# Kernel tuning notes

Hardware: AMD Instinct MI355X
Metric: run time of the kernel (lower is better)

The kernel has to match this reference:

```python
import jax, jax.numpy as jnp
import numpy as np

B, S, E, D, OUT = 128, 128, 256, 256, 64


def setup_inputs() -> dict:
    key = jax.random.key(0)
    ks = jax.random.split(key, 10)
    w = lambda k, shp, s=0.05: (jax.random.normal(k, shp, dtype=jnp.float32) * s)
    return {
        "input_encoded": jax.random.normal(ks[0], (B, S, E), dtype=jnp.float32),
        "y_history": jax.random.normal(ks[1], (B, S, OUT), dtype=jnp.float32),
        "h0": jax.random.normal(ks[2], (B, D), dtype=jnp.float32) * 0.1,
        "c0": jax.random.normal(ks[3], (B, D), dtype=jnp.float32) * 0.1,
        "attn_W1": w(ks[4], (2 * D + E, E)),
        "attn_b1": jnp.zeros((E,), jnp.float32),
        "attn_w2": w(ks[5], (E,)),
        "attn_b2": jnp.zeros((1,), jnp.float32),
        "lstm_Wih": w(ks[6], (OUT, 4 * D)),
        "lstm_Whh": w(ks[7], (D, 4 * D)),
        "lstm_bih": jnp.zeros((4 * D,), jnp.float32),
        "lstm_bhh": jnp.zeros((4 * D,), jnp.float32),
        "fc_W": w(ks[8], (E + OUT, OUT)),
        "fc_b": jnp.zeros((OUT,), jnp.float32),
        "fc_out_W": w(ks[9], (D + E, OUT * S)),
        "fc_out_b": jnp.zeros((OUT * S,), jnp.float32),
    }


def reference(input_encoded, y_history, h0, c0, attn_W1, attn_b1, attn_w2, attn_b2,
              lstm_Wih, lstm_Whh, lstm_bih, lstm_bhh, fc_W, fc_b, fc_out_W, fc_out_b):
    # Split the attn first-layer weight according to the concat order (h, c, enc).
    Wh, Wc, We = attn_W1[:D], attn_W1[D:2 * D], attn_W1[2 * D:]
    # Encoder projection is time-invariant across decoder steps; hoist it.
    enc_proj = jnp.einsum('bse,ef->bsf', input_encoded, We)  # [B,S,E]

    def step(carry, y_t):
        h, c, _ = carry
        hc = h @ Wh + c @ Wc + attn_b1                       # [B,E]
        pre = jnp.tanh(enc_proj + hc[:, None, :])            # [B,S,E]
        scores = pre @ attn_w2 + attn_b2[0]                  # [B,S]
        alpha = jax.nn.softmax(scores, axis=1)
        context = jnp.einsum('bs,bse->be', alpha, input_encoded)  # [B,E]
        y_tilde = jnp.concatenate([context, y_t], axis=1) @ fc_W + fc_b  # [B,OUT]
        gates = y_tilde @ lstm_Wih + lstm_bih + h @ lstm_Whh + lstm_bhh  # [B,4D]
        i, f, g, o = jnp.split(gates, 4, axis=1)  # pytorch gate order i,f,g,o
        c_new = jax.nn.sigmoid(f) * c + jax.nn.sigmoid(i) * jnp.tanh(g)
        h_new = jax.nn.sigmoid(o) * jnp.tanh(c_new)
        return (h_new, c_new, context), None

    y_seq = jnp.transpose(y_history, (1, 0, 2))  # [S,B,OUT]
    (h_T, c_T, context_T), _ = jax.lax.scan(step, (h0, c0, jnp.zeros((B, E), h0.dtype)), y_seq)
    out = jnp.concatenate([h_T, context_T], axis=1) @ fc_out_W + fc_out_b  # [B,OUT*S]
    return out.reshape(-1, S, OUT)
```

## Files before the change

kernel.cpp:

```cpp
#include <hip/hip_runtime.h>

#define BB 128
#define SS 128
#define EE 256
#define DD 256
#define OO 64

#define W1_OFF   0
#define WHH_OFF  196608
#define WIH_OFF  458752
#define FCW_OFF  524288
#define WTOTAL   544768

__device__ __forceinline__ float fsig(float x) { return 1.0f / (1.0f + __expf(-x)); }
__device__ __forceinline__ float ftanh(float x) {
    float t = __expf(-2.0f * fabsf(x));
    float r = (1.0f - t) / (1.0f + t);
    return copysignf(r, x);
}
__device__ __forceinline__ int SWZ(int e) { return (e & ~31) | ((e + 4 * (e >> 5)) & 31); }
__device__ __forceinline__ float bflo(unsigned int u) { return __uint_as_float(u << 16); }
__device__ __forceinline__ float bfhi(unsigned int u) { return __uint_as_float(u & 0xffff0000u); }

__device__ __forceinline__ void fma8(const uint4 w, const float xv, float* acc) {
    acc[0] += xv * bflo(w.x); acc[1] += xv * bfhi(w.x);
    acc[2] += xv * bflo(w.y); acc[3] += xv * bfhi(w.y);
    acc[4] += xv * bflo(w.z); acc[5] += xv * bfhi(w.z);
    acc[6] += xv * bflo(w.w); acc[7] += xv * bfhi(w.w);
}

__global__ __launch_bounds__(256) void conv_kernel(
    const float* __restrict__ W1, const float* __restrict__ Whh,
    const float* __restrict__ Wih, const float* __restrict__ fcW,
    unsigned short* __restrict__ out)
{
    const int idx = blockIdx.x * 256 + threadIdx.x;
    float f;
    if      (idx < WHH_OFF)  f = W1[idx];
    else if (idx < WIH_OFF)  f = Whh[idx - WHH_OFF];
    else if (idx < FCW_OFF)  f = Wih[idx - WIH_OFF];
    else if (idx < WTOTAL)   f = fcW[idx - FCW_OFF];
    else return;
    unsigned int u = __float_as_uint(f);
    u = (u + 0x7fffu + ((u >> 16) & 1u)) >> 16;
    out[idx] = (unsigned short)u;
}

__global__ __launch_bounds__(1024, 4) void scan_kernel(
    const float* __restrict__ inp,
    const float* __restrict__ yhist,
    const float* __restrict__ h0, const float* __restrict__ c0,
    const float* __restrict__ W1f,
    const float* __restrict__ b1, const float* __restrict__ w2, const float* __restrict__ b2,
    const float* __restrict__ bih, const float* __restrict__ bhh,
    const float* __restrict__ fcb,
    const unsigned short* __restrict__ wbf,
    float* __restrict__ hctxT)
{
    __shared__ float sh_inp[SS * 260];
    __shared__ float red1[16 * 256];
    __shared__ float sh_bs[1024];
    __shared__ float sh_h[DD], sh_c[DD];
    __shared__ float sh_hc[EE];
    __shared__ float sh_w2[EE];
    __shared__ float sh_raw[SS];
    __shared__ float sh_ctx[EE];
    __shared__ float sh_y[OO], sh_yt[OO];
    __shared__ float sh_misc[1];

    const int b = blockIdx.x, t = threadIdx.x;
    const float* inp_b = inp + (size_t)b * SS * EE;
    const unsigned short* W1bf  = wbf + W1_OFF;
    const unsigned short* Whhbf = wbf + WHH_OFF;
    const unsigned short* Wihbf = wbf + WIH_OFF;
    const unsigned short* fcWbf = wbf + FCW_OFF;
    const float b2v = b2[0];
    const int lane = t & 63;

    const int e8 = (t & 31) * 8, kc1 = t >> 5;
    const int cg2 = t >> 3, kg2 = t & 7;
    const int s_own = t >> 3, a2 = t & 7, e0 = a2 * 32;
    const int e4 = (t & 63) * 4, sg3 = t >> 6;
    const int kf = (t & 63) * 5, cf = (t >> 6) * 4;

    #pragma unroll
    for (int i = 0; i < 8; ++i) {
        const int idx = i * 1024 + t;
        const int s = idx >> 6, c4 = (idx & 63) * 4;
        *(float4*)&sh_inp[s * 260 + c4] = *(const float4*)(inp_b + (size_t)idx * 4);
    }
    if (t < 256) {
        sh_h[t] = h0[b * 256 + t]; sh_c[t] = c0[b * 256 + t];
        sh_w2[SWZ(t)] = w2[t];
    }
    sh_bs[t] = bih[t] + bhh[t];

    uint4 wih_r[8];
    #pragma unroll
    for (int i = 0; i < 8; ++i)
        wih_r[i] = *(const uint4*)(Wihbf + (size_t)(kg2 * 8 + i) * 1024 + cg2 * 8);
    uint2 fcw_r[5];
    #pragma unroll
    for (int i = 0; i < 5; ++i)
        fcw_r[i] = *(const uint2*)(fcWbf + (kf + i) * 64 + cf);
    __syncthreads();

    float er[32];
    #pragma unroll
    for (int j = 0; j < 32; ++j) er[j] = 0.f;
    {
        const float* We = W1f + 512 * 256;
        for (int kc = 0; kc < 16; ++kc) {
            {
                const int row = t >> 6, c4 = (t & 63) * 4;
                *(float4*)&red1[row * 256 + c4] =
                    *(const float4*)(We + (size_t)(kc * 16 + row) * 256 + c4);
            }
            __syncthreads();
            for (int k = 0; k < 16; ++k) {
                const float xv = sh_inp[s_own * 260 + kc * 16 + k];
                #pragma unroll
                for (int j4 = 0; j4 < 8; ++j4) {
                    float4 w = *(const float4*)&red1[k * 256 + e0 + j4 * 4];
                    er[j4*4+0] += xv * w.x; er[j4*4+1] += xv * w.y;
                    er[j4*4+2] += xv * w.z; er[j4*4+3] += xv * w.w;
                }
            }
            __syncthreads();
        }
        if (t < 256) red1[t] = b1[t];
        __syncthreads();
        #pragma unroll
        for (int j4 = 0; j4 < 8; ++j4) {
            float4 v = *(const float4*)&red1[e0 + j4 * 4];
            er[j4*4+0] += v.x; er[j4*4+1] += v.y; er[j4*4+2] += v.z; er[j4*4+3] += v.w;
        }
        __syncthreads();
    }

    for (int ts = 0; ts < SS; ++ts) {
        if (t < 64) sh_y[t] = yhist[(size_t)b * SS * OO + ts * OO + t];

        {
            float acc[8];
            #pragma unroll
            for (int r = 0; r < 8; ++r) acc[r] = 0.f;
            #pragma unroll 4
            for (int k = kc1 * 16; k < kc1 * 16 + 16; ++k) {
                const float xv = (k < 256) ? sh_h[k] : sh_c[k - 256];
                uint4 w = *(const uint4*)(W1bf + (size_t)k * 256 + e8);
                fma8(w, xv, acc);
            }
            #pragma unroll
            for (int r = 0; r < 8; ++r) acc[r] += __shfl_xor(acc[r], 32);
            if ((t & 32) == 0) {
                *(float4*)&red1[(kc1 >> 1) * 256 + e8]     = make_float4(acc[0], acc[1], acc[2], acc[3]);
                *(float4*)&red1[(kc1 >> 1) * 256 + e8 + 4] = make_float4(acc[4], acc[5], acc[6], acc[7]);
            }
        }
        __syncthreads();
        if (t < 256) {
            float v = 0.f;
            #pragma unroll
            for (int r = 0; r < 16; ++r) v += red1[r * 256 + t];
            sh_hc[SWZ(t)] = v;
        }
        __syncthreads();

        float g[8];
        #pragma unroll
        for (int r = 0; r < 8; ++r) g[r] = 0.f;
        #pragma unroll 8
        for (int i = 0; i < 32; ++i) {
            const int k = kg2 * 32 + ((i + 4 * kg2) & 31);
            const float hv = sh_h[k];
            uint4 w = *(const uint4*)(Whhbf + (size_t)k * 1024 + cg2 * 8);
            fma8(w, hv, g);
        }
        {
            float sacc = 0.f;
            #pragma unroll
            for (int j4 = 0; j4 < 8; ++j4) {
                const int phys = e0 + ((j4 * 4 + 4 * a2) & 31);
                float4 hc4 = *(const float4*)&sh_hc[phys];
                float4 w24 = *(const float4*)&sh_w2[phys];
                sacc += ftanh(er[j4*4+0] + hc4.x) * w24.x;
                sacc += ftanh(er[j4*4+1] + hc4.y) * w24.y;
                sacc += ftanh(er[j4*4+2] + hc4.z) * w24.z;
                sacc += ftanh(er[j4*4+3] + hc4.w) * w24.w;
            }
            sacc += __shfl_xor(sacc, 1);
            sacc += __shfl_xor(sacc, 2);
            sacc += __shfl_xor(sacc, 4);
            if (a2 == 0) sh_raw[s_own] = __expf(sacc + b2v);
        }
        __syncthreads();

        {
            float ax = 0.f, ay = 0.f, az = 0.f, aw = 0.f;
            #pragma unroll
            for (int i = 0; i < 8; ++i) {
                const int s = sg3 * 8 + i;
                const float al = sh_raw[s];
                float4 iv = *(const float4*)&sh_inp[s * 260 + e4];
                ax += al * iv.x; ay += al * iv.y; az += al * iv.z; aw += al * iv.w;
            }
            *(float4*)&red1[sg3 * 256 + e4] = make_float4(ax, ay, az, aw);
        }
        if (t < 64) {
            float v = sh_raw[t] + sh_raw[t + 64];
            #pragma unroll
            for (int m = 32; m > 0; m >>= 1) v += __shfl_xor(v, m);
            if (t == 0) sh_misc[0] = 1.0f / v;
        }
        __syncthreads();
        if (t < 256) {
            float v = 0.f;
            #pragma unroll
            for (int r = 0; r < 16; ++r) v += red1[r * 256 + t];
            v *= sh_misc[0];
            sh_ctx[t] = v;
            if (ts == SS - 1) hctxT[(size_t)(256 + t) * 128 + b] = v;
        }
        __syncthreads();

        {
            float a0 = 0.f, a1 = 0.f, a2v = 0.f, a3 = 0.f;
            #pragma unroll
            for (int i = 0; i < 5; ++i) {
                const int k = kf + i;
                const float val = (k < 256) ? sh_ctx[k] : sh_y[k - 256];
                const uint2 w = fcw_r[i];
                a0  += val * bflo(w.x); a1 += val * bfhi(w.x);
                a2v += val * bflo(w.y); a3 += val * bfhi(w.y);
            }
            #pragma unroll
            for (int m = 1; m < 64; m <<= 1) {
                a0  += __shfl_xor(a0, m);  a1 += __shfl_xor(a1, m);
                a2v += __shfl_xor(a2v, m); a3 += __shfl_xor(a3, m);
            }
            if (lane == 0) {
                float4 r; r.x = a0 + fcb[cf]; r.y = a1 + fcb[cf + 1];
                r.z = a2v + fcb[cf + 2]; r.w = a3 + fcb[cf + 3];
                *(float4*)&sh_yt[cf] = r;
            }
        }
        __syncthreads();

        #pragma unroll
        for (int i = 0; i < 8; ++i) {
            const float yv = sh_yt[kg2 * 8 + i];
            fma8(wih_r[i], yv, g);
        }
        #pragma unroll
        for (int r = 0; r < 8; ++r) {
            g[r] += __shfl_xor(g[r], 1);
            g[r] += __shfl_xor(g[r], 2);
            g[r] += __shfl_xor(g[r], 4);
        }
        if (kg2 == 0) {
            *(float4*)&red1[cg2 * 8]     = make_float4(g[0], g[1], g[2], g[3]);
            *(float4*)&red1[cg2 * 8 + 4] = make_float4(g[4], g[5], g[6], g[7]);
        }
        __syncthreads();
        if (t < 256) {
            const float gi = red1[t]       + sh_bs[t];
            const float gf = red1[256 + t] + sh_bs[256 + t];
            const float gg = red1[512 + t] + sh_bs[512 + t];
            const float go = red1[768 + t] + sh_bs[768 + t];
            const float cn = fsig(gf) * sh_c[t] + fsig(gi) * ftanh(gg);
            sh_c[t] = cn;
            const float hn = fsig(go) * ftanh(cn);
            sh_h[t] = hn;
            if (ts == SS - 1) hctxT[(size_t)t * 128 + b] = hn;
        }
        __syncthreads();
    }
}

__global__ __launch_bounds__(256) void out_gemm(
    const float* __restrict__ AT, const float* __restrict__ W,
    const float* __restrict__ bias, float* __restrict__ out)
{
    __shared__ float Ab[64 * 132];
    __shared__ float Bb[64 * 32];
    const int t = threadIdx.x;
    const int nt = blockIdx.x * 32;
    const int n4 = (t & 7) * 4;
    const int m4 = (t >> 3) * 4;
    float acc[4][4];
    #pragma unroll
    for (int i = 0; i < 4; ++i)
        #pragma unroll
        for (int jj = 0; jj < 4; ++jj) acc[i][jj] = 0.f;

    for (int kc = 0; kc < 8; ++kc) {
        #pragma unroll
        for (int i = 0; i < 8; ++i) {
            const int flat4 = i * 256 + t;
            const int row = flat4 >> 5, mm4 = (flat4 & 31) * 4;
            float4 v = *(const float4*)(AT + (size_t)(kc * 64 + row) * 128 + mm4);
            *(float4*)&Ab[row * 132 + mm4] = v;
        }
        #pragma unroll
        for (int i = 0; i < 2; ++i) {
            const int fl = t + i * 256;
            const int k = fl >> 3, nn4 = (fl & 7) * 4;
            *(float4*)&Bb[k * 32 + nn4] =
                *(const float4*)(W + (size_t)(kc * 64 + k) * 8192 + nt + nn4);
        }
        __syncthreads();
        for (int k = 0; k < 64; ++k) {
            const float4 bv = *(const float4*)&Bb[k * 32 + n4];
            const float4 av = *(const float4*)&Ab[k * 132 + m4];
            acc[0][0] += av.x * bv.x; acc[0][1] += av.x * bv.y; acc[0][2] += av.x * bv.z; acc[0][3] += av.x * bv.w;
            acc[1][0] += av.y * bv.x; acc[1][1] += av.y * bv.y; acc[1][2] += av.y * bv.z; acc[1][3] += av.y * bv.w;
            acc[2][0] += av.z * bv.x; acc[2][1] += av.z * bv.y; acc[2][2] += av.z * bv.z; acc[2][3] += av.z * bv.w;
            acc[3][0] += av.w * bv.x; acc[3][1] += av.w * bv.y; acc[3][2] += av.w * bv.z; acc[3][3] += av.w * bv.w;
        }
        __syncthreads();
    }
    const float4 bb = *(const float4*)(bias + nt + n4);
    #pragma unroll
    for (int i = 0; i < 4; ++i) {
        float4 r;
        r.x = acc[i][0] + bb.x; r.y = acc[i][1] + bb.y;
        r.z = acc[i][2] + bb.z; r.w = acc[i][3] + bb.w;
        *(float4*)(out + (size_t)(m4 + i) * 8192 + nt + n4) = r;
    }
}

extern "C" void kernel_launch(void* const* d_in, const int* in_sizes, int n_in,
                              void* d_out, int out_size, void* d_ws, size_t ws_size,
                              hipStream_t stream) {
    const float* inp = (const float*)d_in[0];
    const float* yh  = (const float*)d_in[1];
    const float* h0  = (const float*)d_in[2];
    const float* c0  = (const float*)d_in[3];
    const float* W1  = (const float*)d_in[4];
    const float* b1  = (const float*)d_in[5];
    const float* w2  = (const float*)d_in[6];
    const float* b2  = (const float*)d_in[7];
    const float* Wih = (const float*)d_in[8];
    const float* Whh = (const float*)d_in[9];
    const float* bih = (const float*)d_in[10];
    const float* bhh = (const float*)d_in[11];
    const float* fcW = (const float*)d_in[12];
    const float* fcb = (const float*)d_in[13];
    const float* foW = (const float*)d_in[14];
    const float* fob = (const float*)d_in[15];

    float* hctxT = (float*)d_ws;
    unsigned short* wbf = (unsigned short*)d_out;

    conv_kernel<<<dim3((WTOTAL + 255) / 256), dim3(256), 0, stream>>>(W1, Whh, Wih, fcW, wbf);
    scan_kernel<<<dim3(BB), dim3(1024), 0, stream>>>(
        inp, yh, h0, c0, W1, b1, w2, b2, bih, bhh, fcb, wbf, hctxT);
    out_gemm<<<dim3(8192 / 32), dim3(256), 0, stream>>>(hctxT, foW, fob, (float*)d_out);
}
```

Measured before the change: 5.483 ms.

## Halve scan block to 512 threads and keep encoder projection in LDS

The recurrent scan kernel now runs with 512 threads per batch row instead of 1024. The precomputed encoder projection plus bias is stored in shared memory rather than held in registers, while the raw input for the context sum is read from global/L2. All four partitions of the matmuls are reworked: deeper per-thread K loops, Wih and fcW weights streamed each step instead of kept in registers, and gate bias folded into the initial accumulators. The aim is fewer threads and shuffles per barrier in this latency-bound serial loop. The cost is more sequential work per thread, an extra barrier in the fc stage, and the context sum now reading inputs from global memory on every step.

```diff
diff --git a/kernel.cpp b/kernel.cpp
--- a/kernel.cpp
+++ b/kernel.cpp
@@ -18,7 +18,6 @@
     float r = (1.0f - t) / (1.0f + t);
     return copysignf(r, x);
 }
-__device__ __forceinline__ int SWZ(int e) { return (e & ~31) | ((e + 4 * (e >> 5)) & 31); }
 __device__ __forceinline__ float bflo(unsigned int u) { return __uint_as_float(u << 16); }
 __device__ __forceinline__ float bfhi(unsigned int u) { return __uint_as_float(u & 0xffff0000u); }
 
@@ -46,7 +45,7 @@
     out[idx] = (unsigned short)u;
 }
 
-__global__ __launch_bounds__(1024, 4) void scan_kernel(
+__global__ __launch_bounds__(512, 2) void scan_kernel(
     const float* __restrict__ inp,
     const float* __restrict__ yhist,
     const float* __restrict__ h0, const float* __restrict__ c0,
@@ -57,16 +56,14 @@
     const unsigned short* __restrict__ wbf,
     float* __restrict__ hctxT)
 {
-    __shared__ float sh_inp[SS * 260];
-    __shared__ float red1[16 * 256];
-    __shared__ float sh_bs[1024];
+    __shared__ float sh_enc[SS * 260];
+    __shared__ float red1a[4096];
+    __shared__ float red1b[1024];
     __shared__ float sh_h[DD], sh_c[DD];
-    __shared__ float sh_hc[EE];
-    __shared__ float sh_w2[EE];
-    __shared__ float sh_raw[SS];
+    __shared__ float sh_hc[EE], sh_w2[EE];
+    __shared__ float sh_raw[132];
     __shared__ float sh_ctx[EE];
     __shared__ float sh_y[OO], sh_yt[OO];
-    __shared__ float sh_misc[1];
 
     const int b = blockIdx.x, t = threadIdx.x;
     const float* inp_b = inp + (size_t)b * SS * EE;
@@ -75,202 +72,195 @@
     const unsigned short* Wihbf = wbf + WIH_OFF;
     const unsigned short* fcWbf = wbf + FCW_OFF;
     const float b2v = b2[0];
-    const int lane = t & 63;
-
-    const int e8 = (t & 31) * 8, kc1 = t >> 5;
-    const int cg2 = t >> 3, kg2 = t & 7;
-    const int s_own = t >> 3, a2 = t & 7, e0 = a2 * 32;
-    const int e4 = (t & 63) * 4, sg3 = t >> 6;
-    const int kf = (t & 63) * 5, cf = (t >> 6) * 4;
-
-    #pragma unroll
-    for (int i = 0; i < 8; ++i) {
-        const int idx = i * 1024 + t;
-        const int s = idx >> 6, c4 = (idx & 63) * 4;
-        *(float4*)&sh_inp[s * 260 + c4] = *(const float4*)(inp_b + (size_t)idx * 4);
-    }
+
+    const int kc1 = t >> 5, e8 = (t & 31) * 8;
+    const int kc2 = t >> 7, j8 = (t & 127) * 8;
+    const int s_own = t >> 2, a2 = t & 3;
+    const int sg3 = t >> 7, c2 = (t & 127) * 2;
+    const int kg = t >> 5, c2b = (t & 31) * 2;
+
     if (t < 256) {
         sh_h[t] = h0[b * 256 + t]; sh_c[t] = c0[b * 256 + t];
-        sh_w2[SWZ(t)] = w2[t];
-    }
-    sh_bs[t] = bih[t] + bhh[t];
-
-    uint4 wih_r[8];
+        sh_w2[t] = w2[t];
+        sh_hc[t] = b1[t];
+    }
+    float bs_r[8];
     #pragma unroll
-    for (int i = 0; i < 8; ++i)
-        wih_r[i] = *(const uint4*)(Wihbf + (size_t)(kg2 * 8 + i) * 1024 + cg2 * 8);
-    uint2 fcw_r[5];
-    #pragma unroll
-    for (int i = 0; i < 5; ++i)
-        fcw_r[i] = *(const uint2*)(fcWbf + (kf + i) * 64 + cf);
+    for (int r = 0; r < 8; ++r) bs_r[r] = 0.f;
+    if (t < 128) {
+        #pragma unroll
+        for (int r = 0; r < 8; ++r) bs_r[r] = bih[t * 8 + r] + bhh[t * 8 + r];
+    }
+    const float fcb_reg = (t < 64) ? fcb[t] : 0.f;
     __syncthreads();
 
-    float er[32];
-    #pragma unroll
-    for (int j = 0; j < 32; ++j) er[j] = 0.f;
     {
+        float4 ec[16];
+        #pragma unroll
+        for (int d = 0; d < 16; ++d) ec[d] = make_float4(0.f, 0.f, 0.f, 0.f);
         const float* We = W1f + 512 * 256;
         for (int kc = 0; kc < 16; ++kc) {
             {
-                const int row = t >> 6, c4 = (t & 63) * 4;
-                *(float4*)&red1[row * 256 + c4] =
-                    *(const float4*)(We + (size_t)(kc * 16 + row) * 256 + c4);
-            }
+                const int row = t >> 5, c8 = (t & 31) * 8;
+                *(float4*)&red1a[row * 256 + c8] =
+                    *(const float4*)(We + (size_t)(kc * 16 + row) * 256 + c8);
+                *(float4*)&red1a[row * 256 + c8 + 4] =
+                    *(const float4*)(We + (size_t)(kc * 16 + row) * 256 + c8 + 4);
+            }
+            float4 xq = *(const float4*)(inp_b + (size_t)s_own * 256 + kc * 16 + a2 * 4);
             __syncthreads();
-            for (int k = 0; k < 16; ++k) {
-                const float xv = sh_inp[s_own * 260 + kc * 16 + k];
+            #pragma unroll
+            for (int q = 0; q < 4; ++q) {
+                const int src = (t & 60) | q;
+                float4 xs;
+                xs.x = __shfl(xq.x, src, 64); xs.y = __shfl(xq.y, src, 64);
+                xs.z = __shfl(xq.z, src, 64); xs.w = __shfl(xq.w, src, 64);
+                const float xv[4] = {xs.x, xs.y, xs.z, xs.w};
                 #pragma unroll
-                for (int j4 = 0; j4 < 8; ++j4) {
-                    float4 w = *(const float4*)&red1[k * 256 + e0 + j4 * 4];
-                    er[j4*4+0] += xv * w.x; er[j4*4+1] += xv * w.y;
-                    er[j4*4+2] += xv * w.z; er[j4*4+3] += xv * w.w;
+                for (int j = 0; j < 4; ++j) {
+                    const int krow = q * 4 + j;
+                    #pragma unroll
+                    for (int d = 0; d < 16; ++d) {
+                        float4 w = *(const float4*)&red1a[krow * 256 + a2 * 64 + d * 4];
+                        ec[d].x += xv[j] * w.x; ec[d].y += xv[j] * w.y;
+                        ec[d].z += xv[j] * w.z; ec[d].w += xv[j] * w.w;
+                    }
                 }
             }
             __syncthreads();
         }
-        if (t < 256) red1[t] = b1[t];
-        __syncthreads();
-        #pragma unroll
-        for (int j4 = 0; j4 < 8; ++j4) {
-            float4 v = *(const float4*)&red1[e0 + j4 * 4];
-            er[j4*4+0] += v.x; er[j4*4+1] += v.y; er[j4*4+2] += v.z; er[j4*4+3] += v.w;
+        #pragma unroll
+        for (int d = 0; d < 16; ++d) {
+            float4 bv = *(const float4*)&sh_hc[a2 * 64 + d * 4];
+            float4 v;
+            v.x = ec[d].x + bv.x; v.y = ec[d].y + bv.y;
+            v.z = ec[d].z + bv.z; v.w = ec[d].w + bv.w;
+            *(float4*)&sh_enc[s_own * 260 + a2 * 64 + d * 4] = v;
         }
         __syncthreads();
     }
 
     for (int ts = 0; ts < SS; ++ts) {
-        if (t < 64) sh_y[t] = yhist[(size_t)b * SS * OO + ts * OO + t];
-
         {
             float acc[8];
             #pragma unroll
             for (int r = 0; r < 8; ++r) acc[r] = 0.f;
-            #pragma unroll 4
-            for (int k = kc1 * 16; k < kc1 * 16 + 16; ++k) {
+            #pragma unroll 8
+            for (int k = kc1 * 32; k < kc1 * 32 + 32; ++k) {
                 const float xv = (k < 256) ? sh_h[k] : sh_c[k - 256];
                 uint4 w = *(const uint4*)(W1bf + (size_t)k * 256 + e8);
                 fma8(w, xv, acc);
             }
-            #pragma unroll
-            for (int r = 0; r < 8; ++r) acc[r] += __shfl_xor(acc[r], 32);
-            if ((t & 32) == 0) {
-                *(float4*)&red1[(kc1 >> 1) * 256 + e8]     = make_float4(acc[0], acc[1], acc[2], acc[3]);
-                *(float4*)&red1[(kc1 >> 1) * 256 + e8 + 4] = make_float4(acc[4], acc[5], acc[6], acc[7]);
-            }
-        }
+            *(float4*)&red1a[kc1 * 256 + e8]     = make_float4(acc[0], acc[1], acc[2], acc[3]);
+            *(float4*)&red1a[kc1 * 256 + e8 + 4] = make_float4(acc[4], acc[5], acc[6], acc[7]);
+        }
+        if (t >= 448) sh_y[t - 448] = yhist[(size_t)b * SS * OO + ts * OO + (t - 448)];
         __syncthreads();
         if (t < 256) {
             float v = 0.f;
             #pragma unroll
-            for (int r = 0; r < 16; ++r) v += red1[r * 256 + t];
-            sh_hc[SWZ(t)] = v;
+            for (int r = 0; r < 16; ++r) v += red1a[r * 256 + t];
+            sh_hc[t] = v;
         }
         __syncthreads();
 
         float g[8];
         #pragma unroll
-        for (int r = 0; r < 8; ++r) g[r] = 0.f;
+        for (int r = 0; r < 8; ++r) g[r] = bs_r[r];
         #pragma unroll 8
-        for (int i = 0; i < 32; ++i) {
-            const int k = kg2 * 32 + ((i + 4 * kg2) & 31);
+        for (int k = kc2 * 64; k < kc2 * 64 + 64; ++k) {
             const float hv = sh_h[k];
-            uint4 w = *(const uint4*)(Whhbf + (size_t)k * 1024 + cg2 * 8);
+            uint4 w = *(const uint4*)(Whhbf + (size_t)k * 1024 + j8);
             fma8(w, hv, g);
         }
         {
             float sacc = 0.f;
             #pragma unroll
-            for (int j4 = 0; j4 < 8; ++j4) {
-                const int phys = e0 + ((j4 * 4 + 4 * a2) & 31);
-                float4 hc4 = *(const float4*)&sh_hc[phys];
-                float4 w24 = *(const float4*)&sh_w2[phys];
-                sacc += ftanh(er[j4*4+0] + hc4.x) * w24.x;
-                sacc += ftanh(er[j4*4+1] + hc4.y) * w24.y;
-                sacc += ftanh(er[j4*4+2] + hc4.z) * w24.z;
-                sacc += ftanh(er[j4*4+3] + hc4.w) * w24.w;
+            for (int d = 0; d < 16; ++d) {
+                const int base = a2 * 64 + ((d * 4 + 16 * a2) & 63);
+                float4 e4v = *(const float4*)&sh_enc[s_own * 260 + base];
+                float4 hc4 = *(const float4*)&sh_hc[base];
+                float4 w24 = *(const float4*)&sh_w2[base];
+                sacc += ftanh(e4v.x + hc4.x) * w24.x;
+                sacc += ftanh(e4v.y + hc4.y) * w24.y;
+                sacc += ftanh(e4v.z + hc4.z) * w24.z;
+                sacc += ftanh(e4v.w + hc4.w) * w24.w;
             }
             sacc += __shfl_xor(sacc, 1);
             sacc += __shfl_xor(sacc, 2);
-            sacc += __shfl_xor(sacc, 4);
             if (a2 == 0) sh_raw[s_own] = __expf(sacc + b2v);
         }
         __syncthreads();
 
         {
-            float ax = 0.f, ay = 0.f, az = 0.f, aw = 0.f;
-            #pragma unroll
-            for (int i = 0; i < 8; ++i) {
-                const int s = sg3 * 8 + i;
+            float ax = 0.f, ay = 0.f;
+            #pragma unroll 4
+            for (int i = 0; i < 32; ++i) {
+                const int s = sg3 * 32 + i;
                 const float al = sh_raw[s];
-                float4 iv = *(const float4*)&sh_inp[s * 260 + e4];
-                ax += al * iv.x; ay += al * iv.y; az += al * iv.z; aw += al * iv.w;
-            }
-            *(float4*)&red1[sg3 * 256 + e4] = make_float4(ax, ay, az, aw);
+                float2 iv = *(const float2*)(inp_b + (size_t)s * 256 + c2);
+                ax += al * iv.x; ay += al * iv.y;
+            }
+            *(float2*)&red1b[sg3 * 256 + c2] = make_float2(ax, ay);
         }
         if (t < 64) {
             float v = sh_raw[t] + sh_raw[t + 64];
             #pragma unroll
             for (int m = 32; m > 0; m >>= 1) v += __shfl_xor(v, m);
-            if (t == 0) sh_misc[0] = 1.0f / v;
+            if (t == 0) sh_raw[128] = 1.0f / v;
         }
         __syncthreads();
         if (t < 256) {
             float v = 0.f;
             #pragma unroll
-            for (int r = 0; r < 16; ++r) v += red1[r * 256 + t];
-            v *= sh_misc[0];
+            for (int r = 0; r < 4; ++r) v += red1b[r * 256 + t];
+            v *= sh_raw[128];
             sh_ctx[t] = v;
             if (ts == SS - 1) hctxT[(size_t)(256 + t) * 128 + b] = v;
         }
         __syncthreads();
 
         {
-            float a0 = 0.f, a1 = 0.f, a2v = 0.f, a3 = 0.f;
-            #pragma unroll
-            for (int i = 0; i < 5; ++i) {
-                const int k = kf + i;
-                const float val = (k < 256) ? sh_ctx[k] : sh_y[k - 256];
-                const uint2 w = fcw_r[i];
-                a0  += val * bflo(w.x); a1 += val * bfhi(w.x);
-                a2v += val * bflo(w.y); a3 += val * bfhi(w.y);
-            }
-            #pragma unroll
-            for (int m = 1; m < 64; m <<= 1) {
-                a0  += __shfl_xor(a0, m);  a1 += __shfl_xor(a1, m);
-                a2v += __shfl_xor(a2v, m); a3 += __shfl_xor(a3, m);
-            }
-            if (lane == 0) {
-                float4 r; r.x = a0 + fcb[cf]; r.y = a1 + fcb[cf + 1];
-                r.z = a2v + fcb[cf + 2]; r.w = a3 + fcb[cf + 3];
-                *(float4*)&sh_yt[cf] = r;
-            }
-        }
-        __syncthreads();
-
-        #pragma unroll
-        for (int i = 0; i < 8; ++i) {
-            const float yv = sh_yt[kg2 * 8 + i];
-            fma8(wih_r[i], yv, g);
-        }
-        #pragma unroll
-        for (int r = 0; r < 8; ++r) {
-            g[r] += __shfl_xor(g[r], 1);
-            g[r] += __shfl_xor(g[r], 2);
-            g[r] += __shfl_xor(g[r], 4);
-        }
-        if (kg2 == 0) {
-            *(float4*)&red1[cg2 * 8]     = make_float4(g[0], g[1], g[2], g[3]);
-            *(float4*)&red1[cg2 * 8 + 4] = make_float4(g[4], g[5], g[6], g[7]);
-        }
-        __syncthreads();
+            float a0 = 0.f, a1 = 0.f;
+            #pragma unroll
+            for (int kk = kg * 20; kk < kg * 20 + 20; ++kk) {
+                const float val = (kk < 256) ? sh_ctx[kk] : sh_y[kk - 256];
+                unsigned int w = *(const unsigned int*)(fcWbf + kk * 64 + c2b);
+                a0 += val * bflo(w); a1 += val * bfhi(w);
+            }
+            *(float2*)&red1b[kg * 64 + c2b] = make_float2(a0, a1);
+        }
+        __syncthreads();
+        if (t < 64) {
+            float v = fcb_reg;
+            #pragma unroll
+            for (int r = 0; r < 16; ++r) v += red1b[r * 64 + t];
+            sh_yt[t] = v;
+        }
+        __syncthreads();
+
+        #pragma unroll
+        for (int i = 0; i < 16; ++i) {
+            const float yv = sh_yt[kc2 * 16 + i];
+            uint4 w = *(const uint4*)(Wihbf + (size_t)(kc2 * 16 + i) * 1024 + j8);
+            fma8(w, yv, g);
+        }
+        *(float4*)&red1a[kc2 * 1024 + j8]     = make_float4(g[0], g[1], g[2], g[3]);
+        *(float4*)&red1a[kc2 * 1024 + j8 + 4] = make_float4(g[4], g[5], g[6], g[7]);
+        __syncthreads();
+
         if (t < 256) {
-            const float gi = red1[t]       + sh_bs[t];
-            const float gf = red1[256 + t] + sh_bs[256 + t];
-            const float gg = red1[512 + t] + sh_bs[512 + t];
-            const float go = red1[768 + t] + sh_bs[768 + t];
-            const float cn = fsig(gf) * sh_c[t] + fsig(gi) * ftanh(gg);
+            float gq[4];
+            #pragma unroll
+            for (int q = 0; q < 4; ++q) {
+                float v = 0.f;
+                #pragma unroll
+                for (int r = 0; r < 4; ++r) v += red1a[r * 1024 + q * 256 + t];
+                gq[q] = v;
+            }
+            const float cn = fsig(gq[1]) * sh_c[t] + fsig(gq[0]) * ftanh(gq[2]);
             sh_c[t] = cn;
-            const float hn = fsig(go) * ftanh(cn);
+            const float hn = fsig(gq[3]) * ftanh(cn);
             sh_h[t] = hn;
             if (ts == SS - 1) hctxT[(size_t)t * 128 + b] = hn;
         }
@@ -354,7 +344,7 @@
     unsigned short* wbf = (unsigned short*)d_out;
 
     conv_kernel<<<dim3((WTOTAL + 255) / 256), dim3(256), 0, stream>>>(W1, Whh, Wih, fcW, wbf);
-    scan_kernel<<<dim3(BB), dim3(1024), 0, stream>>>(
+    scan_kernel<<<dim3(BB), dim3(512), 0, stream>>>(
         inp, yh, h0, c0, W1, b1, w2, b2, bih, bhh, fcb, wbf, hctxT);
     out_gemm<<<dim3(8192 / 32), dim3(256), 0, stream>>>(hctxT, foW, fob, (float*)d_out);
 }
```

After: 5.640 ms. 1.03x slower.
